# Kernel optimization log

Measured on AMD Instinct MI355X. Metric: run time of the kernel, lower is better.

Reference implementation:

```python
import jax, jax.numpy as jnp
import numpy as np
import math

D = 1024; H = 16; HD = D // H; K = 8; NS = 512; G = D // 4
N_IN = D // 5; N_AT = int(D * 0.3); N_OUT = int(D * 0.3)
N_MO = D - N_IN - N_AT - N_OUT
M_IN = 4; M_AT = 128; M_OUT = 16; M_MO = 4; NLM_H = 16
B = 2; T = 512
T_IN = 2; T_MO = 2  # ticks_per_region: input/motor = max(2, K//8)


def _glu(z):
    a, b = jnp.split(z, 2, axis=-1)
    return a * jax.nn.sigmoid(b)


def _rms(x, eps=1e-6):
    return x * jax.lax.rsqrt(jnp.mean(x * x, axis=-1, keepdims=True) + eps)


def _ln(x, g, b, eps=1e-5):
    mu = jnp.mean(x, axis=-1, keepdims=True)
    var = jnp.mean((x - mu) ** 2, axis=-1, keepdims=True)
    return (x - mu) * jax.lax.rsqrt(var + eps) * g + b


def _nlm(tr, w, b):
    # tr: (BT, n, m); w: (m, o, n); b: (n, o) -> GLU-halved (BT, n, o/2)
    return _glu(jnp.einsum('bnm,mon->bno', tr, w) + b)


def _forward(x, Wq, Wk, Wv, Wg, W_in, ln_in_g, ln_in_b, W_at, ln_at_g, ln_at_b,
             W_out, ln_out_g, ln_out_b, W_mo, ln_mo_g, ln_mo_b, tick_embed,
             decay_out, decay_act, Wc, in_w1, in_b1, in_s0, in_tr0,
             at_w1, at_b1, at_w2, at_b2, at_s0, at_tr0,
             out_w1, out_b1, out_w2, out_b2, out_s0, out_tr0,
             mo_w1, mo_b1, mo_s0, mo_tr0,
             idx_out_l, idx_out_r, idx_act_l, idx_act_r):
    Bx, Tx, _ = x.shape
    BT = Bx * Tx
    kk = _rms((x @ Wk).reshape(Bx, Tx, H, HD))
    vv = (x @ Wv).reshape(Bx, Tx, H, HD)
    mask = jnp.tril(jnp.ones((Tx, Tx), dtype=bool))
    scale = 1.0 / math.sqrt(HD)

    state = jnp.broadcast_to(jnp.concatenate([in_s0, at_s0, out_s0, mo_s0]), (BT, D))
    tr_in = jnp.broadcast_to(in_tr0, (BT, N_IN, M_IN))
    tr_at = jnp.broadcast_to(at_tr0, (BT, N_AT, M_AT))
    tr_out = jnp.broadcast_to(out_tr0, (BT, N_OUT, M_OUT))
    tr_mo = jnp.broadcast_to(mo_tr0, (BT, N_MO, M_MO))

    alpha_out = state[:, idx_out_l] * state[:, idx_out_r]
    beta_out = jnp.ones_like(alpha_out)
    alpha_act = state[:, idx_act_l] * state[:, idx_act_r]
    beta_act = jnp.ones_like(alpha_act)
    d_out = jnp.exp(-jnp.clip(decay_out, 0.0, 15.0))
    d_act = jnp.exp(-jnp.clip(decay_act, 0.0, 15.0))

    s_in = state[:, :N_IN]
    s_at = state[:, N_IN:N_IN + N_AT]
    s_out = state[:, N_IN + N_AT:N_IN + N_AT + N_OUT]
    s_mo = state[:, N_IN + N_AT + N_OUT:]

    for t in range(K):  # fixed small tick count
        sync_act = alpha_act * jax.lax.rsqrt(beta_act)
        q = _rms((sync_act @ Wq).reshape(Bx, Tx, H, HD))
        sc = jnp.einsum('bqhd,bkhd->bhqk', q, kk) * scale
        sc = jnp.where(mask, sc, -1e30)
        attn = jnp.einsum('bhqk,bkhd->bqhd', jax.nn.softmax(sc, axis=-1), vv)
        attn = attn.reshape(BT, D) + tick_embed[t]
        gfeat = _glu(state @ Wg)

        if t < T_IN:
            pre = _ln(_glu(jnp.concatenate([attn, s_mo, gfeat], -1) @ W_in), ln_in_g, ln_in_b)
            tr_in = jnp.concatenate([tr_in[:, :, 1:], pre[:, :, None]], -1)
            s_in = _nlm(tr_in, in_w1, in_b1)[..., 0]

        pre = _ln(_glu(jnp.concatenate([s_in, attn], -1) @ W_at), ln_at_g, ln_at_b)
        tr_at = jnp.concatenate([tr_at[:, :, 1:], pre[:, :, None]], -1)
        s_at = _nlm(_nlm(tr_at, at_w1, at_b1), at_w2, at_b2)[..., 0]

        pre = _ln(_glu(jnp.concatenate([s_at, attn, gfeat], -1) @ W_out), ln_out_g, ln_out_b)
        tr_out = jnp.concatenate([tr_out[:, :, 1:], pre[:, :, None]], -1)
        s_out = _nlm(_nlm(tr_out, out_w1, out_b1), out_w2, out_b2)[..., 0]

        if t < T_MO:
            pre = _ln(_glu(jnp.concatenate([s_out, gfeat], -1) @ W_mo), ln_mo_g, ln_mo_b)
            tr_mo = jnp.concatenate([tr_mo[:, :, 1:], pre[:, :, None]], -1)
            s_mo = _nlm(tr_mo, mo_w1, mo_b1)[..., 0]

        state = jnp.concatenate([s_in, s_at, s_out, s_mo], -1)
        alpha_out = d_out * alpha_out + state[:, idx_out_l] * state[:, idx_out_r]
        beta_out = d_out * beta_out + 1.0
        alpha_act = d_act * alpha_act + state[:, idx_act_l] * state[:, idx_act_r]
        beta_act = d_act * beta_act + 1.0

    sync_out = alpha_out * jax.lax.rsqrt(beta_out)
    return (sync_out @ Wc).reshape(Bx, Tx, D)


def setup_inputs():
    key = jax.random.key(0)
    ki = iter(jax.random.split(key, 64))
    s = (3.0 ** 0.5) * (D ** -0.5) * 0.68

    def un(shape, sc):
        return jax.random.uniform(next(ki), shape, jnp.float32, -sc, sc)

    def sl(m, o, n):  # SuperLinear: w (m,o,n), b zeros (n,o)
        sc = 1.0 / math.sqrt(m + o)
        return un((m, o, n), sc), jnp.zeros((n, o), jnp.float32)

    inp = {}
    inp['x'] = jax.random.normal(next(ki), (B, T, D), jnp.float32)
    inp['Wq'] = un((NS, D), s); inp['Wk'] = un((D, D), s); inp['Wv'] = un((D, D), s)
    inp['Wg'] = un((D, 2 * G), s)
    inp['W_in'] = un((D + N_MO + G, 2 * N_IN), s)
    inp['ln_in_g'] = jnp.ones(N_IN); inp['ln_in_b'] = jnp.zeros(N_IN)
    inp['W_at'] = un((N_IN + D, 2 * N_AT), s)
    inp['ln_at_g'] = jnp.ones(N_AT); inp['ln_at_b'] = jnp.zeros(N_AT)
    inp['W_out'] = un((N_AT + D + G, 2 * N_OUT), s)
    inp['ln_out_g'] = jnp.ones(N_OUT); inp['ln_out_b'] = jnp.zeros(N_OUT)
    inp['W_mo'] = un((N_OUT + G, 2 * N_MO), s)
    inp['ln_mo_g'] = jnp.ones(N_MO); inp['ln_mo_b'] = jnp.zeros(N_MO)
    inp['tick_embed'] = jax.random.normal(next(ki), (K, D), jnp.float32) * 0.02
    inp['decay_out'] = jnp.zeros(NS, jnp.float32)
    inp['decay_act'] = jnp.zeros(NS, jnp.float32)
    inp['Wc'] = un((NS, D), s)
    inp['in_w1'], inp['in_b1'] = sl(M_IN, 2, N_IN)
    inp['in_s0'] = un((N_IN,), math.sqrt(1.0 / N_IN))
    inp['in_tr0'] = un((N_IN, M_IN), math.sqrt(1.0 / (N_IN + M_IN)))
    inp['at_w1'], inp['at_b1'] = sl(M_AT, 2 * NLM_H, N_AT)
    inp['at_w2'], inp['at_b2'] = sl(NLM_H, 2, N_AT)
    inp['at_s0'] = un((N_AT,), math.sqrt(1.0 / N_AT))
    inp['at_tr0'] = un((N_AT, M_AT), math.sqrt(1.0 / (N_AT + M_AT)))
    inp['out_w1'], inp['out_b1'] = sl(M_OUT, 2 * NLM_H, N_OUT)
    inp['out_w2'], inp['out_b2'] = sl(NLM_H, 2, N_OUT)
    inp['out_s0'] = un((N_OUT,), math.sqrt(1.0 / N_OUT))
    inp['out_tr0'] = un((N_OUT, M_OUT), math.sqrt(1.0 / (N_OUT + M_OUT)))
    inp['mo_w1'], inp['mo_b1'] = sl(M_MO, 2, N_MO)
    inp['mo_s0'] = un((N_MO,), math.sqrt(1.0 / N_MO))
    inp['mo_tr0'] = un((N_MO, M_MO), math.sqrt(1.0 / (N_MO + M_MO)))
    inp['idx_out_l'] = jax.random.permutation(next(ki), D)[:NS].astype(jnp.int32)
    inp['idx_out_r'] = jax.random.permutation(next(ki), D)[:NS].astype(jnp.int32)
    inp['idx_act_l'] = jax.random.permutation(next(ki), D)[:NS].astype(jnp.int32)
    inp['idx_act_r'] = jax.random.permutation(next(ki), D)[:NS].astype(jnp.int32)
    return inp


def reference(x, Wq, Wk, Wv, Wg, W_in, ln_in_g, ln_in_b, W_at, ln_at_g, ln_at_b,
              W_out, ln_out_g, ln_out_b, W_mo, ln_mo_g, ln_mo_b, tick_embed,
              decay_out, decay_act, Wc, in_w1, in_b1, in_s0, in_tr0,
              at_w1, at_b1, at_w2, at_b2, at_s0, at_tr0,
              out_w1, out_b1, out_w2, out_b2, out_s0, out_tr0,
              mo_w1, mo_b1, mo_s0, mo_tr0,
              idx_out_l, idx_out_r, idx_act_l, idx_act_r):
    return _forward(x, Wq, Wk, Wv, Wg, W_in, ln_in_g, ln_in_b, W_at, ln_at_g, ln_at_b,
                    W_out, ln_out_g, ln_out_b, W_mo, ln_mo_g, ln_mo_b, tick_embed,
                    decay_out, decay_act, Wc, in_w1, in_b1, in_s0, in_tr0,
                    at_w1, at_b1, at_w2, at_b2, at_s0, at_tr0,
                    out_w1, out_b1, out_w2, out_b2, out_s0, out_tr0,
                    mo_w1, mo_b1, mo_s0, mo_tr0,
                    idx_out_l, idx_out_r, idx_act_l, idx_act_r)
```

## Files before the change

kernel.cpp:

```cpp
#include <hip/hip_runtime.h>
#include <hip/hip_bf16.h>
#include <math.h>

typedef __hip_bfloat16 bf16;
typedef short v8s __attribute__((ext_vector_type(8)));
typedef float v4f __attribute__((ext_vector_type(4)));

__device__ __forceinline__ float B2F(bf16 x) { return __bfloat162float(x); }
__device__ __forceinline__ float sigm(float x) { return 1.0f / (1.0f + expf(-x)); }

__device__ __forceinline__ void split2(float v, short& hi, short& lo) {
    unsigned u = __float_as_uint(v);
    hi = (short)(u >> 16);
    float r = v - __uint_as_float(u & 0xFFFF0000u);
    bf16 l = __float2bfloat16(r);
    short ls; __builtin_memcpy(&ls, &l, 2);
    lo = ls;
}

static constexpr int D_    = 1024;
static constexpr int H_    = 16;
static constexpr int KT_   = 8;
static constexpr int NS_   = 512;
static constexpr int G_    = 256;
static constexpr int NIN_  = 204;
static constexpr int NAT_  = 307;
static constexpr int NOUT_ = 307;
static constexpr int NMO_  = 206;
static constexpr int B_    = 2;
static constexpr int T_    = 512;
static constexpr int BT_   = 1024;
static constexpr int NF_   = 41;
static constexpr int NW_   = 9;

static constexpr int LAT_ = 1248;
static constexpr int LOU_ = 1600;
static constexpr int LIN_ = 1504;
static constexpr int LMO_ = 576;

struct CvtArgs { const void* src[NF_]; long long cum[NF_ + 1]; };

__global__ void detect_kernel(const void* probe, int* flag) {
    if (threadIdx.x == 0 && blockIdx.x == 0) {
        unsigned u = *(const unsigned*)probe;
        *flag = (u == 0x3F803F80u) ? 1 : 0;
    }
}

__global__ void cvt_all_kernel(CvtArgs a, float* __restrict__ dst,
                               const int* __restrict__ flag, long long total) {
    long long i0 = ((long long)blockIdx.x * 256 + threadIdx.x) * 4;
    if (i0 >= total) return;
    int lo = 0, hi = NF_;
    while (hi - lo > 1) { int mid = (lo + hi) >> 1; if (a.cum[mid] <= i0) lo = mid; else hi = mid; }
    bool bf = (*flag != 0);
    #pragma unroll
    for (int k = 0; k < 4; ++k) {
        long long i = i0 + k;
        if (i >= total) break;
        if (i >= a.cum[lo + 1]) ++lo;
        long long off = i - a.cum[lo];
        dst[i] = bf ? B2F(((const bf16*)a.src[lo])[off]) : ((const float*)a.src[lo])[off];
    }
}

__global__ void final_any_kernel(const float* __restrict__ src, void* dst,
                                 const int* __restrict__ flag, int n) {
    int i = blockIdx.x * blockDim.x + threadIdx.x;
    if (i >= n) return;
    if (*flag) ((bf16*)dst)[i] = __float2bfloat16(src[i]);
    else       ((float*)dst)[i] = src[i];
}

__global__ void split_pair_kernel(const float* __restrict__ src,
                                  short* __restrict__ dh, short* __restrict__ dl, int n) {
    int i = blockIdx.x * blockDim.x + threadIdx.x;
    if (i >= n) return;
    short h, l; split2(src[i], h, l);
    dh[i] = h; dl[i] = l;
}

__global__ void zeropad_kernel(short* zath, short* zatl, short* zouth, short* zoutl,
                               short* zinh, short* zinl, short* zmoh, short* zmol) {
    int r = blockIdx.x, j = threadIdx.x;
    if (j < 20)      { zath[(size_t)r * LAT_ + 1228 + j] = 0; zatl[(size_t)r * LAT_ + 1228 + j] = 0; }
    else if (j < 33) { zouth[(size_t)r * LOU_ + 1587 + (j - 20)] = 0; zoutl[(size_t)r * LOU_ + 1587 + (j - 20)] = 0; }
    else if (j < 51) { zinh[(size_t)r * LIN_ + 1486 + (j - 33)] = 0; zinl[(size_t)r * LIN_ + 1486 + (j - 33)] = 0; }
    else             { zmoh[(size_t)r * LMO_ + 563 + (j - 51)] = 0; zmol[(size_t)r * LMO_ + 563 + (j - 51)] = 0; }
}

struct TD { int srcOff; long long dstOff; int K, N, ldk; };
struct TDs { TD d[NW_]; };

__global__ __launch_bounds__(256)
void transpose_split_kernel(const float* __restrict__ stage,
                            short* __restrict__ wth, short* __restrict__ wtl, TDs tds)
{
    TD d = tds.d[blockIdx.z];
    if (d.N == 0) return;
    int k0 = blockIdx.y * 32, n0 = blockIdx.x * 32;
    if (k0 >= d.ldk || n0 >= d.N) return;
    __shared__ float T[32][33];
    int r = threadIdx.x >> 5, cc = threadIdx.x & 31;
    const float* src = stage + d.srcOff;
    #pragma unroll
    for (int rr = 0; rr < 4; ++rr) {
        int k = k0 + r + rr * 8;
        int n = n0 + cc;
        T[r + rr * 8][cc] = (k < d.K && n < d.N) ? src[(size_t)k * d.N + n] : 0.f;
    }
    __syncthreads();
    #pragma unroll
    for (int rr = 0; rr < 4; ++rr) {
        int n = n0 + r + rr * 8;
        int k = k0 + cc;
        if (n < d.N) {
            short hi, lo;
            split2(T[cc][r + rr * 8], hi, lo);
            wth[d.dstOff + (size_t)n * d.ldk + k] = hi;
            wtl[d.dstOff + (size_t)n * d.ldk + k] = lo;
        }
    }
}

__global__ __launch_bounds__(256)
void wg_pack_kernel(const float* __restrict__ src,
                    short* __restrict__ wth, short* __restrict__ wtl)
{
    int n0 = blockIdx.x * 32;
    int k0 = blockIdx.y * 32;
    __shared__ float T[32][33];
    int r = threadIdx.x >> 5, cc = threadIdx.x & 31;
    int dng = n0 + cc;
    int nsrc = (dng & 1) ? (G_ + (dng >> 1)) : (dng >> 1);
    #pragma unroll
    for (int rr = 0; rr < 4; ++rr) {
        int k = k0 + r + rr * 8;
        T[r + rr * 8][cc] = src[(size_t)k * 512 + nsrc];
    }
    __syncthreads();
    #pragma unroll
    for (int rr = 0; rr < 4; ++rr) {
        int dn = n0 + r + rr * 8;
        int k = k0 + cc;
        short hi, lo;
        split2(T[cc][r + rr * 8], hi, lo);
        wth[(size_t)dn * 1024 + k] = hi;
        wtl[(size_t)dn * 1024 + k] = lo;
    }
}

__global__ __launch_bounds__(256)
void gemm_mfma_kernel(const short* __restrict__ Ah, const short* __restrict__ Al, int lda_s,
                      const short* __restrict__ WTh, const short* __restrict__ WTl, int ldk,
                      float* __restrict__ C, int ldc, size_t pstride, int N,
                      int KC, int nCh, const int* __restrict__ flag)
{
    __shared__ short AhS[2048], AlS[2048], WhS[2048], WlS[2048];
    const int tid = threadIdx.x;
    const int lane = tid & 63;
    const int wave = tid >> 6;
    const int wm = (wave >> 1) * 32, wn = (wave & 1) * 32;
    const int m0 = blockIdx.y * 64, n0 = blockIdx.x * 64;
    const bool wlo = (*flag == 0);
    v4f acc[2][2] = {};

    const int srow = (tid >> 6) * 16 + (tid & 15);
    const int skoff = ((tid >> 4) & 3) * 8;
    const short* ArowH = Ah + (size_t)(m0 + srow) * lda_s + skoff;
    const short* ArowL = Al + (size_t)(m0 + srow) * lda_s + skoff;
    const int wrow = n0 + srow;
    const bool wv = wrow < N;
    const short* WrowH = WTh + (size_t)(wv ? wrow : 0) * ldk + skoff;
    const short* WrowL = WTl + (size_t)(wv ? wrow : 0) * ldk + skoff;

    const int aoff = ((wm >> 4) * 64 + lane) * 8;
    const int boff = ((wn >> 4) * 64 + lane) * 8;
    const int fr = lane & 15;

    const int c0 = blockIdx.z * KC;
    const int c1 = min(nCh, c0 + KC);
    for (int c = c0; c < c1; ++c) {
        const int k0 = c << 5;
        __syncthreads();
        *(v8s*)&AhS[tid * 8] = *(const v8s*)(ArowH + k0);
        *(v8s*)&AlS[tid * 8] = *(const v8s*)(ArowL + k0);
        {
            v8s wh = {};
            if (wv) wh = *(const v8s*)(WrowH + k0);
            *(v8s*)&WhS[tid * 8] = wh;
            if (wlo) {
                v8s wl = {};
                if (wv) wl = *(const v8s*)(WrowL + k0);
                *(v8s*)&WlS[tid * 8] = wl;
            }
        }
        __syncthreads();
        v8s a_h[2], a_l[2], b_h[2];
        a_h[0] = *(v8s*)&AhS[aoff];
        a_h[1] = *(v8s*)&AhS[aoff + 512];
        a_l[0] = *(v8s*)&AlS[aoff];
        a_l[1] = *(v8s*)&AlS[aoff + 512];
        b_h[0] = *(v8s*)&WhS[boff];
        b_h[1] = *(v8s*)&WhS[boff + 512];
        #pragma unroll
        for (int i = 0; i < 2; ++i)
            #pragma unroll
            for (int j = 0; j < 2; ++j) {
                acc[i][j] = __builtin_amdgcn_mfma_f32_16x16x32_bf16(a_h[i], b_h[j], acc[i][j], 0, 0, 0);
                acc[i][j] = __builtin_amdgcn_mfma_f32_16x16x32_bf16(a_l[i], b_h[j], acc[i][j], 0, 0, 0);
            }
        if (wlo) {
            v8s b_l[2];
            b_l[0] = *(v8s*)&WlS[boff];
            b_l[1] = *(v8s*)&WlS[boff + 512];
            #pragma unroll
            for (int i = 0; i < 2; ++i)
                #pragma unroll
                for (int j = 0; j < 2; ++j)
                    acc[i][j] = __builtin_amdgcn_mfma_f32_16x16x32_bf16(a_h[i], b_l[j], acc[i][j], 0, 0, 0);
        }
    }
    float* Cs = C + (size_t)blockIdx.z * pstride;
    #pragma unroll
    for (int j = 0; j < 2; ++j) {
        int col = n0 + wn + j * 16 + fr;
        if (col < N) {
            #pragma unroll
            for (int i = 0; i < 2; ++i)
                #pragma unroll
                for (int r = 0; r < 4; ++r) {
                    int row = m0 + wm + i * 16 + (lane >> 4) * 4 + r;
                    Cs[(size_t)row * ldc + col] = acc[i][j][r];
                }
        }
    }
}

__global__ void kpack_kernel(const float* __restrict__ kkb,
                             short* __restrict__ kh, short* __restrict__ kl) {
    int idx = blockIdx.x * blockDim.x + threadIdx.x;
    if (idx >= 32 * 512 * 64) return;
    int d = idx & 63;
    int key = (idx >> 6) & 511;
    int bh = idx >> 15;
    int b = bh >> 4, h = bh & 15;
    float v = kkb[(size_t)(b * 512 + key) * 1024 + h * 64 + d];
    short hh, ll; split2(v, hh, ll);
    int kc = key >> 6;
    int t4 = (key & 63) >> 4, f = key & 15;
    int ks = d >> 5, q = (d >> 3) & 3, j = d & 7;
    size_t o = (size_t)bh * 32768 + kc * 4096 + (((t4 * 2 + ks) * 64 + q * 16 + f) * 8) + j;
    kh[o] = hh; kl[o] = ll;
}

__global__ void vpack_kernel(const float* __restrict__ vvb,
                             short* __restrict__ vh, short* __restrict__ vl) {
    int idx = blockIdx.x * blockDim.x + threadIdx.x;
    if (idx >= 32 * 512 * 64) return;
    int d = idx & 63;
    int key = (idx >> 6) & 511;
    int bh = idx >> 15;
    int b = bh >> 4, h = bh & 15;
    float v = vvb[(size_t)(b * 512 + key) * 1024 + h * 64 + d];
    short hh, ll; split2(v, hh, ll);
    int kc = key >> 6;
    int kk2 = key & 63;
    int ks = kk2 >> 5, q = (kk2 >> 3) & 3, j = kk2 & 7;
    int t4 = d >> 4, f = d & 15;
    size_t o = (size_t)bh * 32768 + kc * 4096 + (((t4 * 2 + ks) * 64 + q * 16 + f) * 8) + j;
    vh[o] = hh; vl[o] = ll;
}

__global__ void init_state_kernel(const float* __restrict__ s_in0, const float* __restrict__ s_at0,
                                  const float* __restrict__ s_out0, const float* __restrict__ s_mo0,
                                  float* __restrict__ state,
                                  short* __restrict__ sth, short* __restrict__ stl,
                                  short* __restrict__ zath, short* __restrict__ zatl,
                                  short* __restrict__ zouth, short* __restrict__ zoutl,
                                  short* __restrict__ zinh, short* __restrict__ zinl,
                                  short* __restrict__ zmoh, short* __restrict__ zmol) {
    int idx = blockIdx.x * blockDim.x + threadIdx.x;
    if (idx >= BT_ * D_) return;
    int b = idx >> 10;
    int i = idx & (D_ - 1);
    float v;
    if (i < NIN_) v = s_in0[i];
    else if (i < NIN_ + NAT_) v = s_at0[i - NIN_];
    else if (i < NIN_ + NAT_ + NOUT_) v = s_out0[i - NIN_ - NAT_];
    else v = s_mo0[i - NIN_ - NAT_ - NOUT_];
    state[idx] = v;
    short h, l; split2(v, h, l);
    sth[idx] = h; stl[idx] = l;
    if (i < NIN_) { zath[(size_t)b * LAT_ + i] = h; zatl[(size_t)b * LAT_ + i] = l; }
    else if (i < NIN_ + NAT_) {
        zouth[(size_t)b * LOU_ + (i - NIN_)] = h; zoutl[(size_t)b * LOU_ + (i - NIN_)] = l;
    } else if (i < NIN_ + NAT_ + NOUT_) {
        zmoh[(size_t)b * LMO_ + (i - NIN_ - NAT_)] = h; zmol[(size_t)b * LMO_ + (i - NIN_ - NAT_)] = l;
    } else {
        zinh[(size_t)b * LIN_ + 1024 + (i - NIN_ - NAT_ - NOUT_)] = h;
        zinl[(size_t)b * LIN_ + 1024 + (i - NIN_ - NAT_ - NOUT_)] = l;
    }
}

__global__ void decay_kernel(const float* __restrict__ d_o, const float* __restrict__ d_a,
                             float* __restrict__ eo, float* __restrict__ ea) {
    int j = blockIdx.x * blockDim.x + threadIdx.x;
    if (j >= NS_) return;
    float x = d_o[j]; x = fminf(fmaxf(x, 0.f), 15.f); eo[j] = expf(-x);
    float y = d_a[j]; y = fminf(fmaxf(y, 0.f), 15.f); ea[j] = expf(-y);
}

__global__ void init_sync_kernel(const float* __restrict__ state,
                                 const int* __restrict__ ol, const int* __restrict__ orr,
                                 const int* __restrict__ al, const int* __restrict__ ar,
                                 float* __restrict__ ao, float* __restrict__ bo,
                                 float* __restrict__ aa, float* __restrict__ ba,
                                 short* __restrict__ sbh, short* __restrict__ sbl) {
    int idx = blockIdx.x * blockDim.x + threadIdx.x;
    if (idx >= BT_ * NS_) return;
    int b = idx >> 9;
    int j = idx & (NS_ - 1);
    const float* st = state + (size_t)b * D_;
    float vo = st[ol[j]] * st[orr[j]];
    float va = st[al[j]] * st[ar[j]];
    ao[idx] = vo; bo[idx] = 1.f;
    aa[idx] = va; ba[idx] = 1.f;
    short h, l; split2(va, h, l);
    sbh[idx] = h; sbl[idx] = l;
}

__global__ void syncupd_kernel(const float* __restrict__ state,
                               const float* __restrict__ eo, const float* __restrict__ ea,
                               const int* __restrict__ ol, const int* __restrict__ orr,
                               const int* __restrict__ al, const int* __restrict__ ar,
                               float* __restrict__ ao, float* __restrict__ bo,
                               float* __restrict__ aa, float* __restrict__ ba,
                               short* __restrict__ sbh, short* __restrict__ sbl) {
    int idx = blockIdx.x * blockDim.x + threadIdx.x;
    if (idx >= BT_ * NS_) return;
    int b = idx >> 9;
    int j = idx & (NS_ - 1);
    const float* st = state + (size_t)b * D_;
    float d = eo[j];
    ao[idx] = d * ao[idx] + st[ol[j]] * st[orr[j]];
    bo[idx] = d * bo[idx] + 1.f;
    d = ea[j];
    float a2 = d * aa[idx] + st[al[j]] * st[ar[j]];
    float b2 = d * ba[idx] + 1.f;
    aa[idx] = a2; ba[idx] = b2;
    float v = a2 / sqrtf(b2);
    short h, l; split2(v, h, l);
    sbh[idx] = h; sbl[idx] = l;
}

__global__ void syncact_split_kernel(const float* __restrict__ a, const float* __restrict__ be,
                                     short* __restrict__ oh, short* __restrict__ olo) {
    int idx = blockIdx.x * blockDim.x + threadIdx.x;
    if (idx >= BT_ * NS_) return;
    float v = a[idx] / sqrtf(be[idx]);
    short h, l; split2(v, h, l);
    oh[idx] = h; olo[idx] = l;
}

__global__ void rms64_kernel(float* __restrict__ buf) {
    int r = blockIdx.x * 4 + (threadIdx.x >> 6);
    int lane = threadIdx.x & 63;
    size_t off = (size_t)r * 64 + lane;
    float v = buf[off];
    float ss = v * v;
    #pragma unroll
    for (int o = 32; o > 0; o >>= 1) ss += __shfl_xor(ss, o);
    buf[off] = v * (1.0f / sqrtf(ss * (1.0f / 64.0f) + 1e-6f));
}

__global__ __launch_bounds__(256)
void attn_mfma_kernel(const float* __restrict__ qpart, int qsplits, size_t qps,
                      const short* __restrict__ kh_g, const short* __restrict__ kl_g,
                      const short* __restrict__ vh_g, const short* __restrict__ vl_g,
                      const float* __restrict__ te,
                      short* __restrict__ zath, short* __restrict__ zatl,
                      short* __restrict__ zouth, short* __restrict__ zoutl,
                      short* __restrict__ zinh, short* __restrict__ zinl, int wr_in)
{
    __shared__ short kksh[4096], kksl[4096];
    __shared__ short vtsh[4096], vtsl[4096];
    __shared__ short psh[4][1024], psl[4][1024];

    const int bid = blockIdx.x;
    const int bh = bid >> 3, qbk = bid & 7;
    const int b = bh >> 4, h = bh & 15;
    const int q0 = qbk * 64;
    const int tid = threadIdx.x, w = tid >> 6, lane = tid & 63;
    const int quad = lane >> 4, fr = lane & 15;

    const int qrow = q0 + w * 16 + fr;
    const size_t qoffg = ((size_t)(b * T_ + qrow)) * D_ + h * 64 + quad * 8;
    float qv[16];
    #pragma unroll
    for (int j = 0; j < 8; ++j) { qv[j] = qpart[qoffg + j]; qv[8 + j] = qpart[qoffg + 32 + j]; }
    for (int s = 1; s < qsplits; ++s) {
        const float* qp = qpart + (size_t)s * qps + qoffg;
        #pragma unroll
        for (int j = 0; j < 8; ++j) { qv[j] += qp[j]; qv[8 + j] += qp[32 + j]; }
    }
    float ss = 0.f;
    #pragma unroll
    for (int j = 0; j < 16; ++j) ss += qv[j] * qv[j];
    ss += __shfl_xor(ss, 16);
    ss += __shfl_xor(ss, 32);
    const float qsc = (1.0f / sqrtf(ss * (1.0f / 64.0f) + 1e-6f)) * 0.125f;
    v8s qh[2], ql[2];
    #pragma unroll
    for (int ks = 0; ks < 2; ++ks)
        #pragma unroll
        for (int j = 0; j < 8; ++j) {
            short hh, ll; split2(qv[ks * 8 + j] * qsc, hh, ll);
            qh[ks][j] = hh; ql[ks][j] = ll;
        }

    v4f oacc[4] = {};
    float m_[4], l_[4];
    #pragma unroll
    for (int r = 0; r < 4; ++r) { m_[r] = -INFINITY; l_[r] = 0.f; }

    const size_t kvbase = (size_t)bh * 32768;
    for (int c = 0; c <= qbk; ++c) {
        const size_t cb = kvbase + c * 4096;
        __syncthreads();
        {
            int s0 = tid * 8, s1 = (tid + 256) * 8;
            *(v8s*)&kksh[s0] = *(const v8s*)&kh_g[cb + s0];
            *(v8s*)&kksh[s1] = *(const v8s*)&kh_g[cb + s1];
            *(v8s*)&kksl[s0] = *(const v8s*)&kl_g[cb + s0];
            *(v8s*)&kksl[s1] = *(const v8s*)&kl_g[cb + s1];
            *(v8s*)&vtsh[s0] = *(const v8s*)&vh_g[cb + s0];
            *(v8s*)&vtsh[s1] = *(const v8s*)&vh_g[cb + s1];
            *(v8s*)&vtsl[s0] = *(const v8s*)&vl_g[cb + s0];
            *(v8s*)&vtsl[s1] = *(const v8s*)&vl_g[cb + s1];
        }
        __syncthreads();

        v4f sv[4] = {};
        #pragma unroll
        for (int ks = 0; ks < 2; ++ks) {
            #pragma unroll
            for (int t4 = 0; t4 < 4; ++t4) {
                int so = ((t4 * 2 + ks) * 64 + lane) * 8;
                v8s bh_ = *(v8s*)&kksh[so];
                v8s bl_ = *(v8s*)&kksl[so];
                sv[t4] = __builtin_amdgcn_mfma_f32_16x16x32_bf16(qh[ks], bh_, sv[t4], 0, 0, 0);
                sv[t4] = __builtin_amdgcn_mfma_f32_16x16x32_bf16(ql[ks], bh_, sv[t4], 0, 0, 0);
                sv[t4] = __builtin_amdgcn_mfma_f32_16x16x32_bf16(qh[ks], bl_, sv[t4], 0, 0, 0);
            }
        }

        const int kb = c * 64;
        #pragma unroll
// ... 73 lines not shown
}

__global__ void glu_sum_kernel(const float* __restrict__ p, int S, size_t pstride,
                               short* __restrict__ zouth, short* __restrict__ zoutl,
                               short* __restrict__ zinh, short* __restrict__ zinl,
                               short* __restrict__ zmoh, short* __restrict__ zmol, int wr2) {
    int idx = blockIdx.x * blockDim.x + threadIdx.x;
    if (idx >= BT_ * G_) return;
    int row = idx >> 8, j = idx & 255;
    float a = 0.f, bb = 0.f;
    for (int s = 0; s < S; ++s) {
        const float* pr = p + (size_t)s * pstride + (size_t)row * 512;
        a += pr[2 * j];
        bb += pr[2 * j + 1];
    }
    float gf = a * sigm(bb);
    short hh, ll; split2(gf, hh, ll);
    zouth[(size_t)row * LOU_ + 1331 + j] = hh; zoutl[(size_t)row * LOU_ + 1331 + j] = ll;
    if (wr2) {
        zinh[(size_t)row * LIN_ + 1230 + j] = hh; zinl[(size_t)row * LIN_ + 1230 + j] = ll;
        zmoh[(size_t)row * LMO_ + NOUT_ + j] = hh; zmol[(size_t)row * LMO_ + NOUT_ + j] = ll;
    }
}

__global__ __launch_bounds__(256)
void glu_ln_nlm_big_kernel(const float* __restrict__ z, size_t pstride, int n,
                           const float* __restrict__ g, const float* __restrict__ bb,
                           float* __restrict__ preBase, int t,
                           const float* __restrict__ st, const float* __restrict__ w1,
                           const float* __restrict__ b1, const float* __restrict__ w2,
                           const float* __restrict__ b2,
                           float* __restrict__ state, short* __restrict__ sth,
                           short* __restrict__ stl, int soff, int Mdim,
                           short* __restrict__ czh, short* __restrict__ czl,
                           int ldz, int catoff)
{
    __shared__ float preLDS[320];
    __shared__ float red[256];
    const int row = blockIdx.x;
    const float* zr = z + (size_t)row * 2 * n;
    float v[2];
    float lsum = 0.f;
    {
        int s = 0;
        for (int i = threadIdx.x; i < n; i += 256, ++s) {
            float a = zr[i] + zr[pstride + i] + zr[2 * pstride + i] + zr[3 * pstride + i];
            float gt = zr[n + i] + zr[pstride + n + i] + zr[2 * pstride + n + i] + zr[3 * pstride + n + i];
            float val = a * sigm(gt);
            v[s] = val;
            lsum += val;
        }
    }
    red[threadIdx.x] = lsum;
    __syncthreads();
    for (int sd = 128; sd > 0; sd >>= 1) {
        if (threadIdx.x < sd) red[threadIdx.x] += red[threadIdx.x + sd];
        __syncthreads();
    }
    float mu = red[0] / n;
    __syncthreads();
    float lss = 0.f;
    {
        int s = 0;
        for (int i = threadIdx.x; i < n; i += 256, ++s) { float dv = v[s] - mu; lss += dv * dv; }
    }
    red[threadIdx.x] = lss;
    __syncthreads();
    for (int sd = 128; sd > 0; sd >>= 1) {
        if (threadIdx.x < sd) red[threadIdx.x] += red[threadIdx.x + sd];
        __syncthreads();
    }
    float inv = 1.f / sqrtf(red[0] / n + 1e-5f);
    {
        int s = 0;
        for (int i = threadIdx.x; i < n; i += 256, ++s) {
            float pre = (v[s] - mu) * inv * g[i] + bb[i];
            preLDS[i] = pre;
            preBase[((size_t)t * BT_ + row) * n + i] = pre;
        }
    }
    __syncthreads();
    for (int i = threadIdx.x; i < n; i += 256) {
        float h[32];
        #pragma unroll
        for (int o = 0; o < 32; ++o) h[o] = st[((size_t)t * 32 + o) * n + i] + b1[(size_t)i * 32 + o];
        for (int s = 0; s < t; ++s) {
            float pv = preBase[((size_t)s * BT_ + row) * n + i];
            int mrow = Mdim - 1 - t + s;
            const float* wrow = w1 + (size_t)mrow * 32 * n + i;
            #pragma unroll
            for (int o = 0; o < 32; ++o) h[o] += pv * wrow[(size_t)o * n];
        }
        {
            float pv = preLDS[i];
            const float* wrow = w1 + (size_t)(Mdim - 1) * 32 * n + i;
            #pragma unroll
            for (int o = 0; o < 32; ++o) h[o] += pv * wrow[(size_t)o * n];
        }
        float h20 = b2[i * 2], h21 = b2[i * 2 + 1];
        #pragma unroll
        for (int j = 0; j < 16; ++j) {
            float gv = h[j] * sigm(h[j + 16]);
            h20 += gv * w2[(size_t)(j * 2 + 0) * n + i];
            h21 += gv * w2[(size_t)(j * 2 + 1) * n + i];
        }
        float res = h20 * sigm(h21);
        size_t so = (size_t)row * D_ + soff + i;
        state[so] = res;
        short hh, ll; split2(res, hh, ll);
        sth[so] = hh; stl[so] = ll;
        czh[(size_t)row * ldz + catoff + i] = hh;
        czl[(size_t)row * ldz + catoff + i] = ll;
    }
}

__global__ __launch_bounds__(256)
void glu_ln_nlm_small_kernel(const float* __restrict__ z, size_t pstride, int n,
                             const float* __restrict__ g, const float* __restrict__ bb,
                             float* __restrict__ preBase, int t,
                             const float* __restrict__ tr0, const float* __restrict__ w1,
                             const float* __restrict__ b1,
                             float* __restrict__ state, short* __restrict__ sth,
                             short* __restrict__ stl, int soff,
                             short* __restrict__ czh, short* __restrict__ czl,
                             int ldz, int catoff)
{
    __shared__ float preLDS[320];
    __shared__ float red[256];
    const int row = blockIdx.x;
    const float* zr = z + (size_t)row * 2 * n;
    float v[2];
    float lsum = 0.f;
    {
        int s = 0;
        for (int i = threadIdx.x; i < n; i += 256, ++s) {
            float a = zr[i] + zr[pstride + i] + zr[2 * pstride + i] + zr[3 * pstride + i];
            float gt = zr[n + i] + zr[pstride + n + i] + zr[2 * pstride + n + i] + zr[3 * pstride + n + i];
            float val = a * sigm(gt);
            v[s] = val;
            lsum += val;
        }
    }
    red[threadIdx.x] = lsum;
    __syncthreads();
    for (int sd = 128; sd > 0; sd >>= 1) {
        if (threadIdx.x < sd) red[threadIdx.x] += red[threadIdx.x + sd];
        __syncthreads();
    }
    float mu = red[0] / n;
    __syncthreads();
    float lss = 0.f;
    {
        int s = 0;
        for (int i = threadIdx.x; i < n; i += 256, ++s) { float dv = v[s] - mu; lss += dv * dv; }
    }
    red[threadIdx.x] = lss;
    __syncthreads();
    for (int sd = 128; sd > 0; sd >>= 1) {
        if (threadIdx.x < sd) red[threadIdx.x] += red[threadIdx.x + sd];
        __syncthreads();
    }
    float inv = 1.f / sqrtf(red[0] / n + 1e-5f);
    {
        int s = 0;
        for (int i = threadIdx.x; i < n; i += 256, ++s) {
            float pre = (v[s] - mu) * inv * g[i] + bb[i];
            preLDS[i] = pre;
            preBase[((size_t)t * BT_ + row) * n + i] = pre;
        }
    }
    __syncthreads();
    for (int i = threadIdx.x; i < n; i += 256) {
        float win[4];
        if (t == 0) {
            win[0] = tr0[i * 4 + 1]; win[1] = tr0[i * 4 + 2]; win[2] = tr0[i * 4 + 3];
            win[3] = preLDS[i];
        } else {
            win[0] = tr0[i * 4 + 2]; win[1] = tr0[i * 4 + 3];
            win[2] = preBase[(size_t)row * n + i];
            win[3] = preLDS[i];
        }
        float h0 = b1[i * 2], h1 = b1[i * 2 + 1];
        #pragma unroll
        for (int mm = 0; mm < 4; ++mm) {
            h0 += win[mm] * w1[(size_t)(mm * 2 + 0) * n + i];
            h1 += win[mm] * w1[(size_t)(mm * 2 + 1) * n + i];
        }
        float res = h0 * sigm(h1);
        size_t so = (size_t)row * D_ + soff + i;
        state[so] = res;
        short hh, ll; split2(res, hh, ll);
        sth[so] = hh; stl[so] = ll;
        czh[(size_t)row * ldz + catoff + i] = hh;
        czl[(size_t)row * ldz + catoff + i] = ll;
    }
}

__global__ void static_nlm_kernel(const float* __restrict__ tr0, const float* __restrict__ w1,
                                  float* __restrict__ st, int n, int Mdim)
{
    int idx = blockIdx.x * blockDim.x + threadIdx.x;
    if (idx >= KT_ * n * 32) return;
    int i = idx % n;
    int rest = idx / n;
    int o = rest & 31;
    int t = rest >> 5;
    float s = 0.f;
    for (int j = t + 1; j < Mdim; ++j)
        s += tr0[(size_t)i * Mdim + j] * w1[(size_t)((j - t - 1) * 32 + o) * n + i];
    st[((size_t)t * 32 + o) * n + i] = s;
}

extern "C" void kernel_launch(void* const* d_in, const int* in_sizes, int n_in,
                              void* d_out, int out_size, void* d_ws, size_t ws_size,
                              hipStream_t stream)
{
    const int* idx_ol = (const int*)d_in[41];
    const int* idx_or = (const int*)d_in[42];
    const int* idx_al = (const int*)d_in[43];
    const int* idx_ar = (const int*)d_in[44];

    size_t off = 0;
    auto alloc = [&](size_t ne) {
        float* r = (float*)d_ws + off;
        off += (ne + 63) & ~(size_t)63;
        return r;
    };
    int* flag = (int*)alloc(64);

    CvtArgs ca;
    long long cum = 0;
    for (int i = 0; i < NF_; ++i) { ca.src[i] = d_in[i]; ca.cum[i] = cum; cum += in_sizes[i]; }
    ca.cum[NF_] = cum;
    float* stage = alloc((size_t)cum);
    auto SP = [&](int i) { return (const float*)(stage + ca.cum[i]); };

    const int wIdx[NW_] = {1, 2, 3, 4, 5, 8, 11, 14, 20};
    const int wK[NW_]   = {512, 1024, 1024, 1024, 1486, 1228, 1587, 563, 512};
    const int wN[NW_]   = {1024, 1024, 1024, 512, 408, 614, 614, 412, 1024};
    const int wS[NW_]   = {2, 1, 1, 4, 4, 4, 4, 4, 1};
    int ldkA[NW_];
    long long wOff[NW_];
    long long totS = 0;
    for (int i = 0; i < NW_; ++i) {
        ldkA[i] = (wK[i] + 31) & ~31;
        wOff[i] = totS;
        totS += (long long)wN[i] * ldkA[i];
    }
    short* wtH = (short*)alloc((size_t)(totS + 1) / 2 + 64);
    short* wtL = (short*)alloc((size_t)(totS + 1) / 2 + 64);

    short* xh     = (short*)alloc((size_t)BT_ * D_ / 2 + 64);
    short* xl     = (short*)alloc((size_t)BT_ * D_ / 2 + 64);
    short* sbh    = (short*)alloc((size_t)BT_ * NS_ / 2 + 64);
    short* sbl    = (short*)alloc((size_t)BT_ * NS_ / 2 + 64);
    short* sobh   = (short*)alloc((size_t)BT_ * NS_ / 2 + 64);
    short* sobl   = (short*)alloc((size_t)BT_ * NS_ / 2 + 64);
    short* sth    = (short*)alloc((size_t)BT_ * D_ / 2 + 64);
    short* stl    = (short*)alloc((size_t)BT_ * D_ / 2 + 64);
    short* khp    = (short*)alloc((size_t)32 * 512 * 64 / 2 + 64);
    short* klp    = (short*)alloc((size_t)32 * 512 * 64 / 2 + 64);
    short* vhp    = (short*)alloc((size_t)32 * 512 * 64 / 2 + 64);
    short* vlp    = (short*)alloc((size_t)32 * 512 * 64 / 2 + 64);
    short* zath   = (short*)alloc((size_t)BT_ * LAT_ / 2 + 64);
    short* zatl   = (short*)alloc((size_t)BT_ * LAT_ / 2 + 64);
    short* zouth  = (short*)alloc((size_t)BT_ * LOU_ / 2 + 64);
    short* zoutl  = (short*)alloc((size_t)BT_ * LOU_ / 2 + 64);
    short* zinh   = (short*)alloc((size_t)BT_ * LIN_ / 2 + 64);
    short* zinl   = (short*)alloc((size_t)BT_ * LIN_ / 2 + 64);
    short* zmoh   = (short*)alloc((size_t)BT_ * LMO_ / 2 + 64);
    short* zmol   = (short*)alloc((size_t)BT_ * LMO_ / 2 + 64);

    float* pbuf   = alloc((size_t)4 * BT_ * 1024);
    float* kkb    = alloc((size_t)BT_ * D_);
    float* vvb    = alloc((size_t)BT_ * D_);
    float* state  = alloc((size_t)BT_ * D_);
    float* ao     = alloc((size_t)BT_ * NS_);
    float* bo     = alloc((size_t)BT_ * NS_);
    float* aa     = alloc((size_t)BT_ * NS_);
    float* ba     = alloc((size_t)BT_ * NS_);
    float* eo     = alloc(NS_);
    float* ea     = alloc(NS_);
    float* pre_at = alloc((size_t)KT_ * BT_ * NAT_);
    float* pre_out= alloc((size_t)KT_ * BT_ * NOUT_);
    float* pre_in = alloc((size_t)2 * BT_ * NIN_);
    float* pre_mo = alloc((size_t)2 * BT_ * NMO_);
    float* st_at  = alloc((size_t)KT_ * NAT_ * 32);
    float* st_out = alloc((size_t)KT_ * NOUT_ * 32);
    float* outf   = alloc((size_t)BT_ * D_);
    (void)ws_size; (void)n_in; (void)out_size;

    detect_kernel<<<1, 64, 0, stream>>>(d_in[6], flag);
    cvt_all_kernel<<<(int)((cum / 4 + 255) / 256) + 1, 256, 0, stream>>>(ca, stage, flag, cum);
    zeropad_kernel<<<BT_, 64, 0, stream>>>(zath, zatl, zouth, zoutl, zinh, zinl, zmoh, zmol);
    {
        TDs tds;
        for (int i = 0; i < NW_; ++i) {
            int N = (i == 3) ? 0 : wN[i];
            tds.d[i] = TD{(int)ca.cum[wIdx[i]], wOff[i], wK[i], N, ldkA[i]};
        }
        dim3 g(32, 50, NW_);
        transpose_split_kernel<<<g, 256, 0, stream>>>(stage, wtH, wtL, tds);
    }
    wg_pack_kernel<<<dim3(16, 32), 256, 0, stream>>>(SP(4), wtH + wOff[3], wtL + wOff[3]);

    const float* ln_in_g  = SP(6);
    const float* ln_in_b  = SP(7);
    const float* ln_at_g  = SP(9);
    const float* ln_at_b  = SP(10);
    const float* ln_out_g = SP(12);
    const float* ln_out_b = SP(13);
    const float* ln_mo_g  = SP(15);
    const float* ln_mo_b  = SP(16);
    const float* te       = SP(17);
    const float* dec_o    = SP(18);
    const float* dec_a    = SP(19);
    const float* in_w1    = SP(21);
    const float* in_b1    = SP(22);
    const float* in_s0    = SP(23);
    const float* in_tr0   = SP(24);
    const float* at_w1    = SP(25);
    const float* at_b1    = SP(26);
    const float* at_w2    = SP(27);
    const float* at_b2    = SP(28);
    const float* at_s0    = SP(29);
    const float* at_tr0   = SP(30);
    const float* out_w1   = SP(31);
    const float* out_b1   = SP(32);
    const float* out_w2   = SP(33);
    const float* out_b2   = SP(34);
    const float* out_s0   = SP(35);
    const float* out_tr0  = SP(36);
    const float* mo_w1    = SP(37);
    const float* mo_b1    = SP(38);
    const float* mo_s0    = SP(39);
    const float* mo_tr0   = SP(40);

    auto gemm = [&](const short* Ah, const short* Al, int lda_s, int wi,
                    float* C, int ldc) {
        int nCh = ldkA[wi] >> 5;
        int S = wS[wi];
        int KC = (nCh + S - 1) / S;
        dim3 g((wN[wi] + 63) / 64, BT_ / 64, S);
        gemm_mfma_kernel<<<g, 256, 0, stream>>>(Ah, Al, lda_s, wtH + wOff[wi], wtL + wOff[wi],
                                                ldkA[wi], C, ldc, (size_t)BT_ * ldc,
                                                wN[wi], KC, nCh, flag);
    };

    split_pair_kernel<<<(BT_ * D_) / 256, 256, 0, stream>>>(SP(0), xh, xl, BT_ * D_);
    gemm(xh, xl, 1024, 1, kkb, 1024);
    gemm(xh, xl, 1024, 2, vvb, 1024);
    rms64_kernel<<<BT_ * H_ / 4, 256, 0, stream>>>(kkb);
    kpack_kernel<<<(32 * 512 * 64) / 256, 256, 0, stream>>>(kkb, khp, klp);
    vpack_kernel<<<(32 * 512 * 64) / 256, 256, 0, stream>>>(vvb, vhp, vlp);
    init_state_kernel<<<(BT_ * D_) / 256, 256, 0, stream>>>(in_s0, at_s0, out_s0, mo_s0,
                                                            state, sth, stl,
                                                            zath, zatl, zouth, zoutl,
                                                            zinh, zinl, zmoh, zmol);
    decay_kernel<<<2, 256, 0, stream>>>(dec_o, dec_a, eo, ea);
    init_sync_kernel<<<(BT_ * NS_) / 256, 256, 0, stream>>>(state, idx_ol, idx_or, idx_al, idx_ar,
                                                            ao, bo, aa, ba, sbh, sbl);
    static_nlm_kernel<<<(KT_ * NAT_ * 32 + 255) / 256, 256, 0, stream>>>(at_tr0, at_w1, st_at, NAT_, 128);
    static_nlm_kernel<<<(KT_ * NOUT_ * 32 + 255) / 256, 256, 0, stream>>>(out_tr0, out_w1, st_out, NOUT_, 16);

    for (int t = 0; t < KT_; ++t) {
        gemm(sbh, sbl, 512, 0, pbuf, 1024);
        attn_mfma_kernel<<<256, 256, 0, stream>>>(pbuf, 2, (size_t)BT_ * 1024,
                                                  khp, klp, vhp, vlp, te + (size_t)t * D_,
                                                  zath, zatl, zouth, zoutl, zinh, zinl, (t < 2));
        gemm(sth, stl, 1024, 3, pbuf, 512);
        glu_sum_kernel<<<(BT_ * G_) / 256, 256, 0, stream>>>(pbuf, 4, (size_t)BT_ * 512,
                                                             zouth, zoutl, zinh, zinl,
                                                             zmoh, zmol, (t < 2));
        if (t < 2) {
            gemm(zinh, zinl, LIN_, 4, pbuf, 2 * NIN_);
            glu_ln_nlm_small_kernel<<<BT_, 256, 0, stream>>>(
                pbuf, (size_t)BT_ * 2 * NIN_, NIN_, ln_in_g, ln_in_b, pre_in, t,
                in_tr0, in_w1, in_b1, state, sth, stl, 0, zath, zatl, LAT_, 0);
        }
        gemm(zath, zatl, LAT_, 5, pbuf, 2 * NAT_);
        glu_ln_nlm_big_kernel<<<BT_, 256, 0, stream>>>(
            pbuf, (size_t)BT_ * 2 * NAT_, NAT_, ln_at_g, ln_at_b, pre_at, t,
            st_at, at_w1, at_b1, at_w2, at_b2, state, sth, stl, NIN_, 128,
            zouth, zoutl, LOU_, 0);
        gemm(zouth, zoutl, LOU_, 6, pbuf, 2 * NOUT_);
        glu_ln_nlm_big_kernel<<<BT_, 256, 0, stream>>>(
            pbuf, (size_t)BT_ * 2 * NOUT_, NOUT_, ln_out_g, ln_out_b, pre_out, t,
            st_out, out_w1, out_b1, out_w2, out_b2, state, sth, stl, NIN_ + NAT_, 16,
            zmoh, zmol, LMO_, 0);
        if (t < 2) {
            gemm(zmoh, zmol, LMO_, 7, pbuf, 2 * NMO_);
            glu_ln_nlm_small_kernel<<<BT_, 256, 0, stream>>>(
                pbuf, (size_t)BT_ * 2 * NMO_, NMO_, ln_mo_g, ln_mo_b, pre_mo, t,
                mo_tr0, mo_w1, mo_b1, state, sth, stl, NIN_ + NAT_ + NOUT_,
                zinh, zinl, LIN_, 1024);
        }
        syncupd_kernel<<<(BT_ * NS_) / 256, 256, 0, stream>>>(state, eo, ea, idx_ol, idx_or,
                                                              idx_al, idx_ar, ao, bo, aa, ba, sbh, sbl);
    }

    syncact_split_kernel<<<(BT_ * NS_) / 256, 256, 0, stream>>>(ao, bo, sobh, sobl);
    gemm(sobh, sobl, 512, 8, outf, 1024);
    final_any_kernel<<<(BT_ * D_) / 256, 256, 0, stream>>>(outf, d_out, flag, BT_ * D_);
}
```

Before: 1.885 ms.

## Trim setup: skip staging big weights, fuse K/V GEMM, fuse RMS into kpack

Large inputs (x and the weight matrices) are now read directly from the original buffers with a bf16/fp32 switch, so the conversion pass only stages the small parameters. The K and V projections become one GEMM writing an interleaved 2048-wide buffer. The RMS norm is folded into the K packing kernel, which removes a kernel launch and a read/write pass. The static NLM precompute is restructured to one block per neuron with shared-memory weights and a transposed output layout, and its consumer is updated to match. This relies on the K and V weights being laid out contiguously so the fused GEMM can treat them as one matrix; it mainly trims setup cost, which is small next to the 8-tick loop.

```diff
diff --git a/kernel.cpp b/kernel.cpp
--- a/kernel.cpp
+++ b/kernel.cpp
@@ -16,6 +16,10 @@
     bf16 l = __float2bfloat16(r);
     short ls; __builtin_memcpy(&ls, &l, 2);
     lo = ls;
+}
+
+__device__ __forceinline__ float loadAny(const void* src, size_t off, bool bf) {
+    return bf ? B2F(((const bf16*)src)[off]) : ((const float*)src)[off];
 }
 
 static constexpr int D_    = 1024;
@@ -32,13 +36,14 @@
 static constexpr int BT_   = 1024;
 static constexpr int NF_   = 41;
 static constexpr int NW_   = 9;
+static constexpr int NC_   = 31;
 
 static constexpr int LAT_ = 1248;
 static constexpr int LOU_ = 1600;
 static constexpr int LIN_ = 1504;
 static constexpr int LMO_ = 576;
 
-struct CvtArgs { const void* src[NF_]; long long cum[NF_ + 1]; };
+struct CvtArgs { const void* src[NC_]; long long dstOff[NC_]; long long cum[NC_ + 1]; };
 
 __global__ void detect_kernel(const void* probe, int* flag) {
     if (threadIdx.x == 0 && blockIdx.x == 0) {
@@ -51,7 +56,7 @@
                                const int* __restrict__ flag, long long total) {
     long long i0 = ((long long)blockIdx.x * 256 + threadIdx.x) * 4;
     if (i0 >= total) return;
-    int lo = 0, hi = NF_;
+    int lo = 0, hi = NC_;
     while (hi - lo > 1) { int mid = (lo + hi) >> 1; if (a.cum[mid] <= i0) lo = mid; else hi = mid; }
     bool bf = (*flag != 0);
     #pragma unroll
@@ -60,7 +65,7 @@
         if (i >= total) break;
         if (i >= a.cum[lo + 1]) ++lo;
         long long off = i - a.cum[lo];
-        dst[i] = bf ? B2F(((const bf16*)a.src[lo])[off]) : ((const float*)a.src[lo])[off];
+        dst[a.dstOff[lo] + off] = loadAny(a.src[lo], off, bf);
     }
 }
 
@@ -72,11 +77,12 @@
     else       ((float*)dst)[i] = src[i];
 }
 
-__global__ void split_pair_kernel(const float* __restrict__ src,
-                                  short* __restrict__ dh, short* __restrict__ dl, int n) {
+__global__ void split_x_kernel(const void* __restrict__ src, const int* __restrict__ flag,
+                               short* __restrict__ dh, short* __restrict__ dl, int n) {
     int i = blockIdx.x * blockDim.x + threadIdx.x;
     if (i >= n) return;
-    short h, l; split2(src[i], h, l);
+    float v = loadAny(src, i, *flag != 0);
+    short h, l; split2(v, h, l);
     dh[i] = h; dl[i] = l;
 }
 
@@ -89,11 +95,11 @@
     else             { zmoh[(size_t)r * LMO_ + 563 + (j - 51)] = 0; zmol[(size_t)r * LMO_ + 563 + (j - 51)] = 0; }
 }
 
-struct TD { int srcOff; long long dstOff; int K, N, ldk; };
+struct TD { const void* src; long long dstOff; int K, N, ldk; };
 struct TDs { TD d[NW_]; };
 
 __global__ __launch_bounds__(256)
-void transpose_split_kernel(const float* __restrict__ stage,
+void transpose_split_kernel(const int* __restrict__ flag,
                             short* __restrict__ wth, short* __restrict__ wtl, TDs tds)
 {
     TD d = tds.d[blockIdx.z];
@@ -101,13 +107,15 @@
     int k0 = blockIdx.y * 32, n0 = blockIdx.x * 32;
     if (k0 >= d.ldk || n0 >= d.N) return;
     __shared__ float T[32][33];
+    bool bf = (*flag != 0);
     int r = threadIdx.x >> 5, cc = threadIdx.x & 31;
-    const float* src = stage + d.srcOff;
     #pragma unroll
     for (int rr = 0; rr < 4; ++rr) {
         int k = k0 + r + rr * 8;
         int n = n0 + cc;
-        T[r + rr * 8][cc] = (k < d.K && n < d.N) ? src[(size_t)k * d.N + n] : 0.f;
+        float v = 0.f;
+        if (k < d.K && n < d.N) v = loadAny(d.src, (size_t)k * d.N + n, bf);
+        T[r + rr * 8][cc] = v;
     }
     __syncthreads();
     #pragma unroll
@@ -124,19 +132,20 @@
 }
 
 __global__ __launch_bounds__(256)
-void wg_pack_kernel(const float* __restrict__ src,
+void wg_pack_kernel(const void* __restrict__ src, const int* __restrict__ flag,
                     short* __restrict__ wth, short* __restrict__ wtl)
 {
     int n0 = blockIdx.x * 32;
     int k0 = blockIdx.y * 32;
     __shared__ float T[32][33];
+    bool bf = (*flag != 0);
     int r = threadIdx.x >> 5, cc = threadIdx.x & 31;
     int dng = n0 + cc;
     int nsrc = (dng & 1) ? (G_ + (dng >> 1)) : (dng >> 1);
     #pragma unroll
     for (int rr = 0; rr < 4; ++rr) {
         int k = k0 + r + rr * 8;
-        T[r + rr * 8][cc] = src[(size_t)k * 512 + nsrc];
+        T[r + rr * 8][cc] = loadAny(src, (size_t)k * 512 + nsrc, bf);
     }
     __syncthreads();
     #pragma unroll
@@ -237,24 +246,26 @@
     }
 }
 
-__global__ void kpack_kernel(const float* __restrict__ kkb,
-                             short* __restrict__ kh, short* __restrict__ kl) {
-    int idx = blockIdx.x * blockDim.x + threadIdx.x;
-    if (idx >= 32 * 512 * 64) return;
-    int d = idx & 63;
-    int key = (idx >> 6) & 511;
-    int bh = idx >> 15;
-    int b = bh >> 4, h = bh & 15;
-    float v = kkb[(size_t)(b * 512 + key) * 1024 + h * 64 + d];
+__global__ __launch_bounds__(256)
+void rms_kpack_kernel(const float* __restrict__ kvb,
+                      short* __restrict__ kh, short* __restrict__ kl) {
+    int r = blockIdx.x * 4 + (threadIdx.x >> 6);
+    int d = threadIdx.x & 63;
+    int h = r & 15, key = (r >> 4) & 511, b = r >> 13;
+    float v = kvb[(size_t)(b * 512 + key) * 2048 + h * 64 + d];
+    float ss = v * v;
+    #pragma unroll
+    for (int o = 32; o > 0; o >>= 1) ss += __shfl_xor(ss, o);
+    v *= 1.0f / sqrtf(ss * (1.0f / 64.0f) + 1e-6f);
     short hh, ll; split2(v, hh, ll);
-    int kc = key >> 6;
-    int t4 = (key & 63) >> 4, f = key & 15;
+    int bh = b * 16 + h;
+    int kc = key >> 6, t4 = (key & 63) >> 4, f = key & 15;
     int ks = d >> 5, q = (d >> 3) & 3, j = d & 7;
-    size_t o = (size_t)bh * 32768 + kc * 4096 + (((t4 * 2 + ks) * 64 + q * 16 + f) * 8) + j;
-    kh[o] = hh; kl[o] = ll;
-}
-
-__global__ void vpack_kernel(const float* __restrict__ vvb,
+    size_t o_ = (size_t)bh * 32768 + kc * 4096 + (((t4 * 2 + ks) * 64 + q * 16 + f) * 8) + j;
+    kh[o_] = hh; kl[o_] = ll;
+}
+
+__global__ void vpack_kernel(const float* __restrict__ kvb,
                              short* __restrict__ vh, short* __restrict__ vl) {
     int idx = blockIdx.x * blockDim.x + threadIdx.x;
     if (idx >= 32 * 512 * 64) return;
@@ -262,7 +273,7 @@
     int key = (idx >> 6) & 511;
     int bh = idx >> 15;
     int b = bh >> 4, h = bh & 15;
-    float v = vvb[(size_t)(b * 512 + key) * 1024 + h * 64 + d];
+    float v = kvb[(size_t)(b * 512 + key) * 2048 + 1024 + h * 64 + d];
     short hh, ll; split2(v, hh, ll);
     int kc = key >> 6;
     int kk2 = key & 63;
@@ -363,17 +374,6 @@
     oh[idx] = h; olo[idx] = l;
 }
 
-__global__ void rms64_kernel(float* __restrict__ buf) {
-    int r = blockIdx.x * 4 + (threadIdx.x >> 6);
-    int lane = threadIdx.x & 63;
-    size_t off = (size_t)r * 64 + lane;
-    float v = buf[off];
-    float ss = v * v;
-    #pragma unroll
-    for (int o = 32; o > 0; o >>= 1) ss += __shfl_xor(ss, o);
-    buf[off] = v * (1.0f / sqrtf(ss * (1.0f / 64.0f) + 1e-6f));
-}
-
 __global__ __launch_bounds__(256)
 void attn_mfma_kernel(const float* __restrict__ qpart, int qsplits, size_t qps,
                       const short* __restrict__ kh_g, const short* __restrict__ kl_g,
@@ -613,8 +613,9 @@
     __syncthreads();
     for (int i = threadIdx.x; i < n; i += 256) {
         float h[32];
+        const float* strow = st + ((size_t)t * n + i) * 32;
         #pragma unroll
-        for (int o = 0; o < 32; ++o) h[o] = st[((size_t)t * 32 + o) * n + i] + b1[(size_t)i * 32 + o];
+        for (int o = 0; o < 32; ++o) h[o] = strow[o] + b1[(size_t)i * 32 + o];
         for (int s = 0; s < t; ++s) {
             float pv = preBase[((size_t)s * BT_ + row) * n + i];
             int mrow = Mdim - 1 - t + s;
@@ -727,19 +728,24 @@
     }
 }
 
-__global__ void static_nlm_kernel(const float* __restrict__ tr0, const float* __restrict__ w1,
-                                  float* __restrict__ st, int n, int Mdim)
+__global__ __launch_bounds__(256)
+void static_nlm_kernel(const float* __restrict__ tr0, const float* __restrict__ w1,
+                       float* __restrict__ st, int n, int Mdim)
 {
-    int idx = blockIdx.x * blockDim.x + threadIdx.x;
-    if (idx >= KT_ * n * 32) return;
-    int i = idx % n;
-    int rest = idx / n;
-    int o = rest & 31;
-    int t = rest >> 5;
-    float s = 0.f;
-    for (int j = t + 1; j < Mdim; ++j)
-        s += tr0[(size_t)i * Mdim + j] * w1[(size_t)((j - t - 1) * 32 + o) * n + i];
-    st[((size_t)t * 32 + o) * n + i] = s;
+    __shared__ float ws[127 * 32];
+    __shared__ float trs[128];
+    const int i = blockIdx.x;
+    const int tid = threadIdx.x;
+    const int nw = (Mdim - 1) * 32;
+    for (int idx = tid; idx < nw; idx += 256)
+        ws[idx] = w1[(size_t)idx * n + i];
+    if (tid < Mdim) trs[tid] = tr0[(size_t)i * Mdim + tid];
+    __syncthreads();
+    const int t = tid >> 5, o = tid & 31;
+    float h = 0.f;
+    for (int j = 0; j + t + 1 < Mdim; ++j)
+        h += trs[j + t + 1] * ws[j * 32 + o];
+    st[((size_t)t * n + i) * 32 + o] = h;
 }
 
 extern "C" void kernel_launch(void* const* d_in, const int* in_sizes, int n_in,
@@ -759,12 +765,25 @@
     };
     int* flag = (int*)alloc(64);
 
+    long long fcum[NF_ + 1];
+    fcum[0] = 0;
+    for (int i = 0; i < NF_; ++i) fcum[i + 1] = fcum[i] + in_sizes[i];
+    float* stage = alloc((size_t)fcum[NF_]);
+    auto SP = [&](int i) { return (const float*)(stage + fcum[i]); };
+
+    const int cIdx[NC_] = {6, 7, 9, 10, 12, 13, 15, 16, 17, 18, 19,
+                           21, 22, 23, 24, 25, 26, 27, 28, 29, 30,
+                           31, 32, 33, 34, 35, 36, 37, 38, 39, 40};
     CvtArgs ca;
-    long long cum = 0;
-    for (int i = 0; i < NF_; ++i) { ca.src[i] = d_in[i]; ca.cum[i] = cum; cum += in_sizes[i]; }
-    ca.cum[NF_] = cum;
-    float* stage = alloc((size_t)cum);
-    auto SP = [&](int i) { return (const float*)(stage + ca.cum[i]); };
+    long long ccum = 0;
+    for (int i = 0; i < NC_; ++i) {
+        int gi = cIdx[i];
+        ca.src[i] = d_in[gi];
+        ca.dstOff[i] = fcum[gi];
+        ca.cum[i] = ccum;
+        ccum += in_sizes[gi];
+    }
+    ca.cum[NC_] = ccum;
 
     const int wIdx[NW_] = {1, 2, 3, 4, 5, 8, 11, 14, 20};
     const int wK[NW_]   = {512, 1024, 1024, 1024, 1486, 1228, 1587, 563, 512};
@@ -803,8 +822,7 @@
     short* zmol   = (short*)alloc((size_t)BT_ * LMO_ / 2 + 64);
 
     float* pbuf   = alloc((size_t)4 * BT_ * 1024);
-    float* kkb    = alloc((size_t)BT_ * D_);
-    float* vvb    = alloc((size_t)BT_ * D_);
+    float* kvb    = alloc((size_t)BT_ * 2048);
     float* state  = alloc((size_t)BT_ * D_);
     float* ao     = alloc((size_t)BT_ * NS_);
     float* bo     = alloc((size_t)BT_ * NS_);
@@ -822,18 +840,18 @@
     (void)ws_size; (void)n_in; (void)out_size;
 
     detect_kernel<<<1, 64, 0, stream>>>(d_in[6], flag);
-    cvt_all_kernel<<<(int)((cum / 4 + 255) / 256) + 1, 256, 0, stream>>>(ca, stage, flag, cum);
+    cvt_all_kernel<<<(int)((ccum / 4 + 255) / 256) + 1, 256, 0, stream>>>(ca, stage, flag, ccum);
     zeropad_kernel<<<BT_, 64, 0, stream>>>(zath, zatl, zouth, zoutl, zinh, zinl, zmoh, zmol);
     {
         TDs tds;
         for (int i = 0; i < NW_; ++i) {
             int N = (i == 3) ? 0 : wN[i];
-            tds.d[i] = TD{(int)ca.cum[wIdx[i]], wOff[i], wK[i], N, ldkA[i]};
+            tds.d[i] = TD{d_in[wIdx[i]], wOff[i], wK[i], N, ldkA[i]};
         }
         dim3 g(32, 50, NW_);
-        transpose_split_kernel<<<g, 256, 0, stream>>>(stage, wtH, wtL, tds);
-    }
-    wg_pack_kernel<<<dim3(16, 32), 256, 0, stream>>>(SP(4), wtH + wOff[3], wtL + wOff[3]);
+        transpose_split_kernel<<<g, 256, 0, stream>>>(flag, wtH, wtL, tds);
+    }
+    wg_pack_kernel<<<dim3(16, 32), 256, 0, stream>>>(d_in[4], flag, wtH + wOff[3], wtL + wOff[3]);
 
     const float* ln_in_g  = SP(6);
     const float* ln_in_b  = SP(7);
@@ -878,12 +896,14 @@
                                                 wN[wi], KC, nCh, flag);
     };
 
-    split_pair_kernel<<<(BT_ * D_) / 256, 256, 0, stream>>>(SP(0), xh, xl, BT_ * D_);
-    gemm(xh, xl, 1024, 1, kkb, 1024);
-    gemm(xh, xl, 1024, 2, vvb, 1024);
-    rms64_kernel<<<BT_ * H_ / 4, 256, 0, stream>>>(kkb);
-    kpack_kernel<<<(32 * 512 * 64) / 256, 256, 0, stream>>>(kkb, khp, klp);
-    vpack_kernel<<<(32 * 512 * 64) / 256, 256, 0, stream>>>(vvb, vhp, vlp);
+    split_x_kernel<<<(BT_ * D_) / 256, 256, 0, stream>>>(d_in[0], flag, xh, xl, BT_ * D_);
+    {
+        dim3 g(2048 / 64, BT_ / 64, 1);
+        gemm_mfma_kernel<<<g, 256, 0, stream>>>(xh, xl, 1024, wtH + wOff[1], wtL + wOff[1],
+                                                1024, kvb, 2048, 0, 2048, 32, 32, flag);
+    }
+    rms_kpack_kernel<<<(B_ * T_ * H_) / 4, 256, 0, stream>>>(kvb, khp, klp);
+    vpack_kernel<<<(32 * 512 * 64) / 256, 256, 0, stream>>>(kvb, vhp, vlp);
     init_state_kernel<<<(BT_ * D_) / 256, 256, 0, stream>>>(in_s0, at_s0, out_s0, mo_s0,
                                                             state, sth, stl,
                                                             zath, zatl, zouth, zoutl,
@@ -891,8 +911,8 @@
     decay_kernel<<<2, 256, 0, stream>>>(dec_o, dec_a, eo, ea);
     init_sync_kernel<<<(BT_ * NS_) / 256, 256, 0, stream>>>(state, idx_ol, idx_or, idx_al, idx_ar,
                                                             ao, bo, aa, ba, sbh, sbl);
-    static_nlm_kernel<<<(KT_ * NAT_ * 32 + 255) / 256, 256, 0, stream>>>(at_tr0, at_w1, st_at, NAT_, 128);
-    static_nlm_kernel<<<(KT_ * NOUT_ * 32 + 255) / 256, 256, 0, stream>>>(out_tr0, out_w1, st_out, NOUT_, 16);
+    static_nlm_kernel<<<NAT_, 256, 0, stream>>>(at_tr0, at_w1, st_at, NAT_, 128);
+    static_nlm_kernel<<<NOUT_, 256, 0, stream>>>(out_tr0, out_w1, st_out, NOUT_, 16);
 
     for (int t = 0; t < KT_; ++t) {
         gemm(sbh, sbl, 512, 0, pbuf, 1024);
```

Result: faster. 1.816 ms (-3.7%).
